# Optimization experiments

Hardware: AMD Instinct MI355X
Metric: run time of the kernel (lower is better)

The kernel has to match this reference:

```python
import jax, jax.numpy as jnp
import numpy as np
from jax import lax

B, T, D, H = 2, 2048, 512, 8
HD = D // H
EPS = 1e-5


def _layernorm(x, g, b):
    m = jnp.mean(x, axis=-1, keepdims=True)
    v = jnp.var(x, axis=-1, keepdims=True)
    return (x - m) / jnp.sqrt(v + EPS) * g + b


def setup_inputs() -> dict:
    key = jax.random.key(0)
    ks = jax.random.split(key, 16)
    s = 0.02
    return {
        "x": jax.random.normal(ks[0], (B, T, D), jnp.float32),
        "pe": jax.random.normal(ks[1], (B, T, D), jnp.float32),
        "conv_w": jax.random.normal(ks[2], (D, D, 3), jnp.float32) * s,   # OIH
        "conv_b": jnp.zeros((D,), jnp.float32),
        "in_proj_w": jax.random.normal(ks[3], (3 * D, D), jnp.float32) * s,
        "in_proj_b": jnp.zeros((3 * D,), jnp.float32),
        "out_proj_w": jax.random.normal(ks[4], (D, D), jnp.float32) * s,
        "out_proj_b": jnp.zeros((D,), jnp.float32),
        "ln1_g": jnp.ones((D,), jnp.float32),
        "ln1_b": jnp.zeros((D,), jnp.float32),
        "w1": jax.random.normal(ks[5], (2 * D, D), jnp.float32) * s,
        "b1": jnp.zeros((2 * D,), jnp.float32),
        "w2": jax.random.normal(ks[6], (D, 2 * D), jnp.float32) * s,
        "b2": jnp.zeros((D,), jnp.float32),
        "ln2_g": jnp.ones((D,), jnp.float32),
        "ln2_b": jnp.zeros((D,), jnp.float32),
    }


def reference(x, pe, conv_w, conv_b, in_proj_w, in_proj_b, out_proj_w,
              out_proj_b, ln1_g, ln1_b, w1, b1, w2, b2, ln2_g, ln2_b):
    Bv, Tv, Dv = x.shape
    window = max(Tv // 4, 1)
    half = window // 2
    idx = jnp.arange(Tv)
    blocked = jnp.abs(idx[:, None] - idx[None, :]) > half  # [T, T]
    mask = jnp.where(blocked, -jnp.inf, 0.0).astype(x.dtype)

    # Conv1d on values: x [B,T,D] -> [B,D,T], kernel3 pad1, back to [B,T,D]
    xT = jnp.transpose(x, (0, 2, 1))
    v_in = lax.conv_general_dilated(xT, conv_w, window_strides=(1,),
                                    padding=((1, 1),),
                                    dimension_numbers=("NCH", "OIH", "NCH"))
    v_in = jnp.transpose(v_in + conv_b[None, :, None], (0, 2, 1))

    # MultiheadAttention(q=x, k=x, v=v_in)
    Wq, Wk, Wv = jnp.split(in_proj_w, 3, axis=0)
    bq, bk, bv = jnp.split(in_proj_b, 3, axis=0)
    q = (x @ Wq.T + bq).reshape(Bv, Tv, H, HD).transpose(0, 2, 1, 3)
    k = (x @ Wk.T + bk).reshape(Bv, Tv, H, HD).transpose(0, 2, 1, 3)
    v = (v_in @ Wv.T + bv).reshape(Bv, Tv, H, HD).transpose(0, 2, 1, 3)

    scores = jnp.einsum("bhqd,bhkd->bhqk", q, k) / np.sqrt(HD).astype(x.dtype)
    scores = scores + mask[None, None]
    attn = jax.nn.softmax(scores, axis=-1)
    ctx = jnp.einsum("bhqk,bhkd->bhqd", attn, v)
    ctx = ctx.transpose(0, 2, 1, 3).reshape(Bv, Tv, Dv)
    attn_out = ctx @ out_proj_w.T + out_proj_b

    h = _layernorm(x + attn_out, ln1_g, ln1_b)
    ffn = jax.nn.relu(h @ w1.T + b1) @ w2.T + b2
    return _layernorm(h + ffn, ln2_g, ln2_b)
```

## Files before the change

kernel.cpp:

```cpp
#include <hip/hip_runtime.h>
#include <cstdint>
#include <cstddef>

static constexpr int kT  = 2048;
static constexpr int kD  = 512;
static constexpr int kB  = 2;
static constexpr int kN  = kB * kT;

using short8 = __attribute__((ext_vector_type(8))) short;
using f32x4  = __attribute__((ext_vector_type(4))) float;
typedef unsigned short ushort;

__device__ inline ushort f2bf(float f) {
  uint32_t u = __builtin_bit_cast(uint32_t, f);
  uint32_t r = (u + 0x7FFFu + ((u >> 16) & 1u)) >> 16;
  return (ushort)r;
}

#define GLOAD_LDS16(g, l)                                         \
  __builtin_amdgcn_global_load_lds(                               \
      (const __attribute__((address_space(1))) void*)(g),         \
      (__attribute__((address_space(3))) void*)(l), 16, 0, 0)

__global__ __launch_bounds__(256) void prep_kernel(
    const float* __restrict__ x,   const float* __restrict__ ipw,
    const float* __restrict__ opw, const float* __restrict__ w1,
    const float* __restrict__ w2,  const float* __restrict__ cw,
    ushort* __restrict__ xb,   ushort* __restrict__ ipwb,
    ushort* __restrict__ opwb, ushort* __restrict__ w1b,
    ushort* __restrict__ w2b,  ushort* __restrict__ wcat,
    ushort* __restrict__ acat)
{
  constexpr int C0 = 524288;
  constexpr int C1 = C0 + 196608;
  constexpr int C2 = C1 + 65536;
  constexpr int C3 = C2 + 131072;
  constexpr int C4 = C3 + 131072;
  constexpr int C5 = C4 + 262144;
  constexpr int C6 = C5 + 786432;

  auto cast4 = [](const float* in, ushort* out, int u) {
    float4 v = *reinterpret_cast<const float4*>(&in[(size_t)u * 4]);
    ushort o[4] = {f2bf(v.x), f2bf(v.y), f2bf(v.z), f2bf(v.w)};
    *reinterpret_cast<uint2*>(&out[(size_t)u * 4]) =
        *reinterpret_cast<uint2*>(o);
  };

  for (int u = blockIdx.x * 256 + threadIdx.x; u < C6; u += gridDim.x * 256) {
    if (u < C0) {
      cast4(x, xb, u);
    } else if (u < C1) {
      cast4(ipw, ipwb, u - C0);
    } else if (u < C2) {
      cast4(opw, opwb, u - C1);
    } else if (u < C3) {
      cast4(w1, w1b, u - C2);
    } else if (u < C4) {
      cast4(w2, w2b, u - C3);
    } else if (u < C5) {
      int t = u - C4;
      int o = t >> 9, i = t & 511;
      const float* src = &cw[(size_t)(o * kD + i) * 3];
      ushort* dst = &wcat[(size_t)o * (3 * kD) + i];
#pragma unroll
      for (int tap = 0; tap < 3; ++tap) dst[tap * kD] = f2bf(src[tap]);
    } else {
      int t = u - C5;
      int m = t / 192, r = t - m * 192;
      int tap = r >> 6, i8 = r & 63;
      int tib = (m & (kT - 1)) + tap - 1;
      ushort ob[8] = {0, 0, 0, 0, 0, 0, 0, 0};
      if (tib >= 0 && tib < kT) {
        const float* src = &x[(size_t)(m + tap - 1) * kD + i8 * 8];
        float4 v0 = *reinterpret_cast<const float4*>(src);
        float4 v1 = *reinterpret_cast<const float4*>(src + 4);
        ob[0] = f2bf(v0.x); ob[1] = f2bf(v0.y); ob[2] = f2bf(v0.z);
        ob[3] = f2bf(v0.w); ob[4] = f2bf(v1.x); ob[5] = f2bf(v1.y);
        ob[6] = f2bf(v1.z); ob[7] = f2bf(v1.w);
      }
      *reinterpret_cast<uint4*>(
          &acat[(size_t)m * (3 * kD) + tap * kD + i8 * 8]) =
          *reinterpret_cast<uint4*>(ob);
    }
  }
}

template <typename OutT, int RELU>
__global__ __launch_bounds__(256) void gemm_bf16(
    const ushort* __restrict__ A, const ushort* __restrict__ W,
    const float* __restrict__ bias, OutT* __restrict__ C,
    int M, int Nn, int K)
{
  __shared__ __align__(16) ushort As[2][64 * 128];
  __shared__ __align__(16) ushort Bs[2][64 * 128];
  const int tid = threadIdx.x;
  const int lane = tid & 63, w = tid >> 6;
  const int wr = w >> 1, wc = w & 1;
  const int m0 = blockIdx.x * 64, n0 = blockIdx.y * 64;
  const int fr = lane & 15, g = lane >> 4;

  f32x4 acc[2][2];
#pragma unroll
  for (int i = 0; i < 2; ++i)
#pragma unroll
    for (int j = 0; j < 2; ++j) acc[i][j] = {0.f, 0.f, 0.f, 0.f};

  const ushort* gA[4];
  const ushort* gB[4];
#pragma unroll
  for (int i = 0; i < 4; ++i) {
    int u = i * 256 + tid;
    int row = u >> 4, c = (u & 15) ^ (row & 7);
    gA[i] = A + (size_t)(m0 + row) * K + c * 8;
    gB[i] = W + (size_t)(n0 + row) * K + c * 8;
  }

  auto stage = [&](int buf, int k0) {
#pragma unroll
    for (int i = 0; i < 4; ++i)
      GLOAD_LDS16(gA[i] + k0, &As[buf][(i * 256 + w * 64) * 8]);
#pragma unroll
    for (int i = 0; i < 4; ++i)
      GLOAD_LDS16(gB[i] + k0, &Bs[buf][(i * 256 + w * 64) * 8]);
  };

  const int nt = K >> 7;
  stage(0, 0);
  for (int t = 0; t < nt; ++t) {
    const int buf = t & 1;
    if (t + 1 < nt) {
      stage(buf ^ 1, (t + 1) << 7);
      asm volatile("s_waitcnt vmcnt(8)" ::: "memory");
    } else {
      asm volatile("s_waitcnt vmcnt(0)" ::: "memory");
    }
    __builtin_amdgcn_s_barrier();
    __builtin_amdgcn_sched_barrier(0);

    short8 a[2][4], b[2][4];
#pragma unroll
    for (int m = 0; m < 2; ++m)
#pragma unroll
      for (int kc = 0; kc < 4; ++kc) {
        int r = wr * 32 + m * 16 + fr;
        a[m][kc] = *reinterpret_cast<const short8*>(
            &As[buf][(r * 16 + ((kc * 4 + g) ^ (r & 7))) * 8]);
      }
#pragma unroll
    for (int n = 0; n < 2; ++n)
#pragma unroll
      for (int kc = 0; kc < 4; ++kc) {
        int r = wc * 32 + n * 16 + fr;
        b[n][kc] = *reinterpret_cast<const short8*>(
            &Bs[buf][(r * 16 + ((kc * 4 + g) ^ (r & 7))) * 8]);
      }
#pragma unroll
    for (int m = 0; m < 2; ++m)
#pragma unroll
      for (int n = 0; n < 2; ++n)
#pragma unroll
        for (int kc = 0; kc < 4; ++kc)
          acc[m][n] = __builtin_amdgcn_mfma_f32_16x16x32_bf16(
              a[m][kc], b[n][kc], acc[m][n], 0, 0, 0);

    __builtin_amdgcn_sched_barrier(0);
    __builtin_amdgcn_s_barrier();
  }

  float bv[2];
#pragma unroll
  for (int n = 0; n < 2; ++n) bv[n] = bias[n0 + wc * 32 + n * 16 + fr];
#pragma unroll
  for (int m = 0; m < 2; ++m) {
#pragma unroll
    for (int j = 0; j < 4; ++j) {
      int row = m0 + wr * 32 + m * 16 + g * 4 + j;
#pragma unroll
      for (int n = 0; n < 2; ++n) {
        int col = n0 + wc * 32 + n * 16 + fr;
        float v = acc[m][n][j] + bv[n];
        if (RELU) v = fmaxf(v, 0.f);
        if constexpr (sizeof(OutT) == 2)
          C[(size_t)row * Nn + col] = (OutT)f2bf(v);
        else
          C[(size_t)row * Nn + col] = (OutT)v;
      }
    }
  }
}

__global__ __launch_bounds__(256) void attn_mfma(
    const ushort* __restrict__ QK, const ushort* __restrict__ V,
    ushort* __restrict__ Ctx)
{
  constexpr int PAD = 72;
  __shared__ __align__(16) ushort Ks[2][64 * 64];
  __shared__ __align__(16) ushort Vt[2][64][PAD];
  __shared__ __align__(16) ushort Pl[4][16][PAD];
  const int tid = threadIdx.x;
  const int lane = tid & 63, w = tid >> 6;
  const int l15 = lane & 15, g = lane >> 4;
  const int bh = blockIdx.y;
  const int b = bh >> 3, h = bh & 7;
  const int r0 = blockIdx.x * 64;
  const int rowbase = b * kT;
  const int qrow0 = r0 + w * 16;
  const int t_lo = max(r0 - 256, 0);
  const int t_last = min(r0 + 256, kT - 64);
  const int ntiles = ((t_last - t_lo) >> 6) + 1;

  short8 qf[2];
  {
    const size_t qb = (size_t)(rowbase + qrow0 + l15) * 1024 + h * 64 + g * 8;
    qf[0] = *reinterpret_cast<const short8*>(&QK[qb]);
    qf[1] = *reinterpret_cast<const short8*>(&QK[qb + 32]);
  }

  uint4 vreg[2];
  auto issueK = [&](int buf, int j0) {
#pragma unroll
    for (int c = 0; c < 2; ++c) {
      int u = c * 256 + tid;
      int row = u >> 3;
      int col8 = (u & 7) ^ (row & 7);
      const ushort* src =
          &QK[(size_t)(rowbase + j0 + row) * 1024 + 512 + h * 64 + col8 * 8];
      GLOAD_LDS16(src, &Ks[buf][(c * 256 + w * 64) * 8]);
    }
  };
  auto issueV = [&](int j0) {
#pragma unroll
    for (int i = 0; i < 2; ++i)
      vreg[i] = *reinterpret_cast<const uint4*>(
          &V[(size_t)(rowbase + j0 + lane) * 512 + h * 64 + (w + 4 * i) * 8]);
  };
  auto writeV = [&](int buf) {
#pragma unroll
    for (int i = 0; i < 2; ++i) {
      int dg = w + 4 * i;
      ushort tmp[8];
      *reinterpret_cast<uint4*>(tmp) = vreg[i];
#pragma unroll
      for (int e = 0; e < 8; ++e) Vt[buf][dg * 8 + e][lane] = tmp[e];
    }
  };

  f32x4 acc[4];
#pragma unroll
  for (int d = 0; d < 4; ++d) acc[d] = {0.f, 0.f, 0.f, 0.f};
  float mrun[4] = {-1e30f, -1e30f, -1e30f, -1e30f};
  float lrun[4] = {0.f, 0.f, 0.f, 0.f};

  issueK(0, t_lo);
  issueV(t_lo);
  asm volatile("s_waitcnt vmcnt(0)" ::: "memory");
  writeV(0);
  __syncthreads();

  for (int tt = 0; tt < ntiles; ++tt) {
    const int buf = tt & 1;
    const int j0 = t_lo + tt * 64;
    if (tt + 1 < ntiles) {
      issueK(buf ^ 1, j0 + 64);
      issueV(j0 + 64);
    }

    f32x4 s[4];
#pragma unroll
    for (int n = 0; n < 4; ++n) {
      f32x4 z = {0.f, 0.f, 0.f, 0.f};
#pragma unroll
      for (int kc = 0; kc < 2; ++kc) {
        int row = n * 16 + l15;
        int unit = row * 8 + ((kc * 4 + g) ^ (row & 7));
        short8 kb = *reinterpret_cast<const short8*>(&Ks[buf][unit * 8]);
        z = __builtin_amdgcn_mfma_f32_16x16x32_bf16(qf[kc], kb, z, 0, 0, 0);
      }
      s[n] = z;
    }
#pragma unroll
    for (int n = 0; n < 4; ++n)
#pragma unroll
      for (int j = 0; j < 4; ++j) {
        int col = j0 + n * 16 + l15;
        int qr = qrow0 + g * 4 + j;
        int dlt = col - qr;
        float v = s[n][j] * 0.125f;
        s[n][j] = (dlt > 256 || dlt < -256) ? -1e30f : v;
      }
    float pn[4][4];
    float sold[4];
#pragma unroll
    for (int j = 0; j < 4; ++j) {
      float mx = fmaxf(fmaxf(s[0][j], s[1][j]), fmaxf(s[2][j], s[3][j]));
      mx = fmaxf(mx, __shfl_xor(mx, 1));
      mx = fmaxf(mx, __shfl_xor(mx, 2));
      mx = fmaxf(mx, __shfl_xor(mx, 4));
      mx = fmaxf(mx, __shfl_xor(mx, 8));
      float mnew = fmaxf(mrun[j], mx);
      float sc = __expf(mrun[j] - mnew);
      mrun[j] = mnew;
      sold[j] = sc;
      float rs = 0.f;
#pragma unroll
      for (int n = 0; n < 4; ++n) {
        float p = __expf(s[n][j] - mnew);
        pn[n][j] = p;
        rs += p;
      }
      rs += __shfl_xor(rs, 1);
      rs += __shfl_xor(rs, 2);
      rs += __shfl_xor(rs, 4);
      rs += __shfl_xor(rs, 8);
      lrun[j] = lrun[j] * sc + rs;
    }
#pragma unroll
    for (int d = 0; d < 4; ++d)
#pragma unroll
      for (int j = 0; j < 4; ++j) acc[d][j] *= sold[j];
#pragma unroll
    for (int n = 0; n < 4; ++n)
#pragma unroll
      for (int j = 0; j < 4; ++j)
        Pl[w][g * 4 + j][n * 16 + l15] = f2bf(pn[n][j]);
    asm volatile("s_waitcnt lgkmcnt(0)" ::: "memory");
    __builtin_amdgcn_sched_barrier(0);

    short8 pa[2];
    pa[0] = *reinterpret_cast<const short8*>(&Pl[w][l15][g * 8]);
    pa[1] = *reinterpret_cast<const short8*>(&Pl[w][l15][32 + g * 8]);
#pragma unroll
    for (int d = 0; d < 4; ++d) {
#pragma unroll
      for (int kc = 0; kc < 2; ++kc) {
        short8 vb = *reinterpret_cast<const short8*>(
            &Vt[buf][d * 16 + l15][kc * 32 + g * 8]);
        acc[d] = __builtin_amdgcn_mfma_f32_16x16x32_bf16(pa[kc], vb, acc[d], 0, 0, 0);
      }
    }

    if (tt + 1 < ntiles) {
      asm volatile("s_waitcnt vmcnt(0)" ::: "memory");
      writeV(buf ^ 1);
    }
    __syncthreads();
  }

  float inv[4];
#pragma unroll
  for (int j = 0; j < 4; ++j) inv[j] = 1.f / lrun[j];
#pragma unroll
  for (int d = 0; d < 4; ++d)
#pragma unroll
    for (int j = 0; j < 4; ++j) {
      float v = acc[d][j] * inv[j];
      Ctx[(size_t)(rowbase + qrow0 + g * 4 + j) * 512 + h * 64 + d * 16 + l15] =
          f2bf(v);
    }
}

__global__ __launch_bounds__(256) void ln_kernel(
    const float* __restrict__ A, const float* __restrict__ Bq,
    const float* __restrict__ G, const float* __restrict__ Bt,
    float* __restrict__ Out, ushort* __restrict__ OutB)
{
  const int lane = threadIdx.x & 63;
  const int wv = threadIdx.x >> 6;
  const int row = blockIdx.x * 4 + wv;
  const size_t base = (size_t)row * kD + lane * 8;

  float4 a0 = *reinterpret_cast<const float4*>(&A[base]);
  float4 a1 = *reinterpret_cast<const float4*>(&A[base + 4]);
  float4 b0 = *reinterpret_cast<const float4*>(&Bq[base]);
  float4 b1 = *reinterpret_cast<const float4*>(&Bq[base + 4]);
  float x[8] = {a0.x + b0.x, a0.y + b0.y, a0.z + b0.z, a0.w + b0.w,
                a1.x + b1.x, a1.y + b1.y, a1.z + b1.z, a1.w + b1.w};
  float s = 0.f, ss = 0.f;
#pragma unroll
  for (int i = 0; i < 8; ++i) { s += x[i]; ss += x[i] * x[i]; }
#pragma unroll
  for (int o = 1; o < 64; o <<= 1) {
    s += __shfl_xor(s, o, 64);
    ss += __shfl_xor(ss, o, 64);
  }
  const float mean = s * (1.f / kD);
  const float var = ss * (1.f / kD) - mean * mean;
  const float rs = rsqrtf(var + 1e-5f);

  const int c = lane * 8;
  float4 g0 = *reinterpret_cast<const float4*>(&G[c]);
  float4 g1 = *reinterpret_cast<const float4*>(&G[c + 4]);
  float4 t0 = *reinterpret_cast<const float4*>(&Bt[c]);
  float4 t1 = *reinterpret_cast<const float4*>(&Bt[c + 4]);
  float y[8];
  y[0] = (x[0] - mean) * rs * g0.x + t0.x;
  y[1] = (x[1] - mean) * rs * g0.y + t0.y;
  y[2] = (x[2] - mean) * rs * g0.z + t0.z;
  y[3] = (x[3] - mean) * rs * g0.w + t0.w;
  y[4] = (x[4] - mean) * rs * g1.x + t1.x;
  y[5] = (x[5] - mean) * rs * g1.y + t1.y;
  y[6] = (x[6] - mean) * rs * g1.z + t1.z;
  y[7] = (x[7] - mean) * rs * g1.w + t1.w;
  *reinterpret_cast<float4*>(&Out[base]) = {y[0], y[1], y[2], y[3]};
  *reinterpret_cast<float4*>(&Out[base + 4]) = {y[4], y[5], y[6], y[7]};
  if (OutB) {
    ushort ob[8];
#pragma unroll
    for (int i = 0; i < 8; ++i) ob[i] = f2bf(y[i]);
    *reinterpret_cast<uint4*>(&OutB[base]) = *reinterpret_cast<uint4*>(ob);
  }
}

extern "C" void kernel_launch(void* const* d_in, const int* in_sizes, int n_in,
                              void* d_out, int out_size, void* d_ws, size_t ws_size,
                              hipStream_t stream)
{
  const float* x   = (const float*)d_in[0];
  const float* cw  = (const float*)d_in[2];
  const float* cb  = (const float*)d_in[3];
  const float* ipw = (const float*)d_in[4];
  const float* ipb = (const float*)d_in[5];
  const float* opw = (const float*)d_in[6];
  const float* opb = (const float*)d_in[7];
  const float* g1  = (const float*)d_in[8];
  const float* b1n = (const float*)d_in[9];
  const float* w1  = (const float*)d_in[10];
  const float* bb1 = (const float*)d_in[11];
  const float* w2  = (const float*)d_in[12];
  const float* bb2 = (const float*)d_in[13];
  const float* g2  = (const float*)d_in[14];
  const float* b2n = (const float*)d_in[15];
  float* out = (float*)d_out;

  char* p = (char*)d_ws;
  auto take = [&](size_t bytes) {
    char* q = p; p += (bytes + 255) & ~size_t(255); return q;
  };
  ushort* xb    = (ushort*)take((size_t)kN * kD * 2);
  char*  acat_r =          take((size_t)kN * 3 * kD * 2);
  ushort* acat  = (ushort*)acat_r;
  ushort* wcat  = (ushort*)take((size_t)kD * 3 * kD * 2);
  ushort* ipwb  = (ushort*)take((size_t)3 * kD * kD * 2);
  ushort* opwb  = (ushort*)take((size_t)kD * kD * 2);
  ushort* w1b   = (ushort*)take((size_t)2 * kD * kD * 2);
  ushort* w2b   = (ushort*)take((size_t)2 * kD * kD * 2);
  ushort* convo = (ushort*)take((size_t)kN * kD * 2);
  char*  qk_r   =          take((size_t)kN * 2 * kD * 2);
  ushort* qkb   = (ushort*)qk_r;
  ushort* vbb   = (ushort*)take((size_t)kN * kD * 2);
  ushort* ctx   = (ushort*)take((size_t)kN * kD * 2);
  float* hbuf   = (float*)take((size_t)kN * kD * 4);
  ushort* hb    = (ushort*)take((size_t)kN * kD * 2);
  float* attno  = (float*)acat_r;
  ushort* f1    = (ushort*)qk_r;
  float* f2     = (float*)acat_r;

  dim3 blk(256);
  prep_kernel<<<dim3(2048), blk, 0, stream>>>(
      x, ipw, opw, w1, w2, cw, xb, ipwb, opwb, w1b, w2b, wcat, acat);

  gemm_bf16<ushort, 0><<<dim3(kN / 64, kD / 64), blk, 0, stream>>>(
      acat, wcat, cb, convo, kN, kD, 3 * kD);
  gemm_bf16<ushort, 0><<<dim3(kN / 64, 1024 / 64), blk, 0, stream>>>(
      xb, ipwb, ipb, qkb, kN, 1024, kD);
  gemm_bf16<ushort, 0><<<dim3(kN / 64, kD / 64), blk, 0, stream>>>(
      convo, ipwb + (size_t)1024 * kD, ipb + 1024, vbb, kN, kD, kD);
  attn_mfma<<<dim3(kT / 64, kB * 8), blk, 0, stream>>>(qkb, vbb, ctx);
  gemm_bf16<float, 0><<<dim3(kN / 64, kD / 64), blk, 0, stream>>>(
      ctx, opwb, opb, attno, kN, kD, kD);
  ln_kernel<<<dim3(kN / 4), blk, 0, stream>>>(x, attno, g1, b1n, hbuf, hb);
  gemm_bf16<ushort, 1><<<dim3(kN / 64, 1024 / 64), blk, 0, stream>>>(
      hb, w1b, bb1, f1, kN, 1024, kD);
  gemm_bf16<float, 0><<<dim3(kN / 64, kD / 64), blk, 0, stream>>>(
      f1, w2b, bb2, f2, kN, kD, 2 * kD);
  ln_kernel<<<dim3(kN / 4), blk, 0, stream>>>(hbuf, f2, g2, b2n, out, nullptr);
}
```

Measured before the change: 204.5 us.

## Fold conv weights into V projection and fuse QK and V GEMMs

```diff
diff --git a/kernel.cpp b/kernel.cpp
--- a/kernel.cpp
+++ b/kernel.cpp
@@ -22,22 +22,29 @@
       (const __attribute__((address_space(1))) void*)(g),         \
       (__attribute__((address_space(3))) void*)(l), 16, 0, 0)
 
+struct __align__(16) SmemGemm {
+  ushort As[2][64 * 128];
+  ushort Bs[2][64 * 128];
+};
+
 __global__ __launch_bounds__(256) void prep_kernel(
     const float* __restrict__ x,   const float* __restrict__ ipw,
     const float* __restrict__ opw, const float* __restrict__ w1,
     const float* __restrict__ w2,  const float* __restrict__ cw,
+    const float* __restrict__ cb,
     ushort* __restrict__ xb,   ushort* __restrict__ ipwb,
     ushort* __restrict__ opwb, ushort* __restrict__ w1b,
-    ushort* __restrict__ w2b,  ushort* __restrict__ wcat,
-    ushort* __restrict__ acat)
+    ushort* __restrict__ w2b,  ushort* __restrict__ wct,
+    ushort* __restrict__ acat, float* __restrict__ bvpart)
 {
   constexpr int C0 = 524288;
   constexpr int C1 = C0 + 196608;
   constexpr int C2 = C1 + 65536;
   constexpr int C3 = C2 + 131072;
   constexpr int C4 = C3 + 131072;
-  constexpr int C5 = C4 + 262144;
+  constexpr int C5 = C4 + 786432;
   constexpr int C6 = C5 + 786432;
+  constexpr int C7 = C6 + 4096;
 
   auto cast4 = [](const float* in, ushort* out, int u) {
     float4 v = *reinterpret_cast<const float4*>(&in[(size_t)u * 4]);
@@ -46,7 +53,7 @@
         *reinterpret_cast<uint2*>(o);
   };
 
-  for (int u = blockIdx.x * 256 + threadIdx.x; u < C6; u += gridDim.x * 256) {
+  for (int u = blockIdx.x * 256 + threadIdx.x; u < C7; u += gridDim.x * 256) {
     if (u < C0) {
       cast4(x, xb, u);
     } else if (u < C1) {
@@ -59,12 +66,10 @@
       cast4(w2, w2b, u - C3);
     } else if (u < C5) {
       int t = u - C4;
-      int o = t >> 9, i = t & 511;
-      const float* src = &cw[(size_t)(o * kD + i) * 3];
-      ushort* dst = &wcat[(size_t)o * (3 * kD) + i];
-#pragma unroll
-      for (int tap = 0; tap < 3; ++tap) dst[tap * kD] = f2bf(src[tap]);
-    } else {
+      int ti = t >> 9, c = t & 511;
+      int tap = ti >> 9, i = ti & 511;
+      wct[(size_t)ti * 512 + c] = f2bf(cw[((size_t)c * 512 + i) * 3 + tap]);
+    } else if (u < C6) {
       int t = u - C5;
       int m = t / 192, r = t - m * 192;
       int tap = r >> 6, i8 = r & 63;
@@ -81,22 +86,28 @@
       *reinterpret_cast<uint4*>(
           &acat[(size_t)m * (3 * kD) + tap * kD + i8 * 8]) =
           *reinterpret_cast<uint4*>(ob);
+    } else {
+      int t = u - C6;
+      int o = t >> 3, seg = t & 7;
+      float s = 0.f;
+      const float* wr = &ipw[(size_t)(1024 + o) * kD + seg * 64];
+      const float* cr = &cb[seg * 64];
+#pragma unroll 8
+      for (int c = 0; c < 64; ++c) s = fmaf(wr[c], cr[c], s);
+      bvpart[t] = s;
     }
   }
 }
 
 template <typename OutT, int RELU>
-__global__ __launch_bounds__(256) void gemm_bf16(
+__device__ void gemm_tile(SmemGemm& S,
     const ushort* __restrict__ A, const ushort* __restrict__ W,
     const float* __restrict__ bias, OutT* __restrict__ C,
-    int M, int Nn, int K)
-{
-  __shared__ __align__(16) ushort As[2][64 * 128];
-  __shared__ __align__(16) ushort Bs[2][64 * 128];
+    int Nn, int K, int m0, int n0)
+{
   const int tid = threadIdx.x;
   const int lane = tid & 63, w = tid >> 6;
   const int wr = w >> 1, wc = w & 1;
-  const int m0 = blockIdx.x * 64, n0 = blockIdx.y * 64;
   const int fr = lane & 15, g = lane >> 4;
 
   f32x4 acc[2][2];
@@ -118,10 +129,10 @@
   auto stage = [&](int buf, int k0) {
 #pragma unroll
     for (int i = 0; i < 4; ++i)
-      GLOAD_LDS16(gA[i] + k0, &As[buf][(i * 256 + w * 64) * 8]);
+      GLOAD_LDS16(gA[i] + k0, &S.As[buf][(i * 256 + w * 64) * 8]);
 #pragma unroll
     for (int i = 0; i < 4; ++i)
-      GLOAD_LDS16(gB[i] + k0, &Bs[buf][(i * 256 + w * 64) * 8]);
+      GLOAD_LDS16(gB[i] + k0, &S.Bs[buf][(i * 256 + w * 64) * 8]);
   };
 
   const int nt = K >> 7;
@@ -137,22 +148,22 @@
     __builtin_amdgcn_s_barrier();
     __builtin_amdgcn_sched_barrier(0);
 
-    short8 a[2][4], b[2][4];
+    short8 av[2][4], bv[2][4];
 #pragma unroll
     for (int m = 0; m < 2; ++m)
 #pragma unroll
       for (int kc = 0; kc < 4; ++kc) {
         int r = wr * 32 + m * 16 + fr;
-        a[m][kc] = *reinterpret_cast<const short8*>(
-            &As[buf][(r * 16 + ((kc * 4 + g) ^ (r & 7))) * 8]);
+        av[m][kc] = *reinterpret_cast<const short8*>(
+            &S.As[buf][(r * 16 + ((kc * 4 + g) ^ (r & 7))) * 8]);
       }
 #pragma unroll
     for (int n = 0; n < 2; ++n)
 #pragma unroll
       for (int kc = 0; kc < 4; ++kc) {
         int r = wc * 32 + n * 16 + fr;
-        b[n][kc] = *reinterpret_cast<const short8*>(
-            &Bs[buf][(r * 16 + ((kc * 4 + g) ^ (r & 7))) * 8]);
+        bv[n][kc] = *reinterpret_cast<const short8*>(
+            &S.Bs[buf][(r * 16 + ((kc * 4 + g) ^ (r & 7))) * 8]);
       }
 #pragma unroll
     for (int m = 0; m < 2; ++m)
@@ -161,15 +172,16 @@
 #pragma unroll
         for (int kc = 0; kc < 4; ++kc)
           acc[m][n] = __builtin_amdgcn_mfma_f32_16x16x32_bf16(
-              a[m][kc], b[n][kc], acc[m][n], 0, 0, 0);
+              av[m][kc], bv[n][kc], acc[m][n], 0, 0, 0);
 
     __builtin_amdgcn_sched_barrier(0);
     __builtin_amdgcn_s_barrier();
   }
 
-  float bv[2];
-#pragma unroll
-  for (int n = 0; n < 2; ++n) bv[n] = bias[n0 + wc * 32 + n * 16 + fr];
+  float bb[2];
+#pragma unroll
+  for (int n = 0; n < 2; ++n)
+    bb[n] = bias ? bias[n0 + wc * 32 + n * 16 + fr] : 0.f;
 #pragma unroll
   for (int m = 0; m < 2; ++m) {
 #pragma unroll
@@ -178,7 +190,7 @@
 #pragma unroll
       for (int n = 0; n < 2; ++n) {
         int col = n0 + wc * 32 + n * 16 + fr;
-        float v = acc[m][n][j] + bv[n];
+        float v = acc[m][n][j] + bb[n];
         if (RELU) v = fmaxf(v, 0.f);
         if constexpr (sizeof(OutT) == 2)
           C[(size_t)row * Nn + col] = (OutT)f2bf(v);
@@ -186,6 +198,53 @@
           C[(size_t)row * Nn + col] = (OutT)v;
       }
     }
+  }
+}
+
+template <typename OutT, int RELU>
+__global__ __launch_bounds__(256) void gemm_bf16(
+    const ushort* __restrict__ A, const ushort* __restrict__ W,
+    const float* __restrict__ bias, OutT* __restrict__ C, int Nn, int K)
+{
+  __shared__ SmemGemm S;
+  gemm_tile<OutT, RELU>(S, A, W, bias, C, Nn, K,
+                        blockIdx.x * 64, blockIdx.y * 64);
+}
+
+__global__ __launch_bounds__(256) void wprep_kernel(
+    const ushort* __restrict__ ipwb, const ushort* __restrict__ wct,
+    ushort* __restrict__ wveff, const float* __restrict__ ipb,
+    const float* __restrict__ bvpart, float* __restrict__ bveff)
+{
+  __shared__ SmemGemm S;
+  const int bid = blockIdx.x;
+  const int m0 = (bid / 24) * 64, n0 = (bid % 24) * 64;
+  gemm_tile<ushort, 0>(S, ipwb + (size_t)1024 * kD, wct, nullptr, wveff,
+                       3 * kD, kD, m0, n0);
+  if (bid < 2) {
+    int o = bid * 256 + threadIdx.x;
+    float s = ipb[1024 + o];
+#pragma unroll
+    for (int e = 0; e < 8; ++e) s += bvpart[o * 8 + e];
+    bveff[o] = s;
+  }
+}
+
+__global__ __launch_bounds__(256) void qkv_kernel(
+    const ushort* __restrict__ xb, const ushort* __restrict__ acat,
+    const ushort* __restrict__ ipwb, const float* __restrict__ ipb,
+    const ushort* __restrict__ wveff, const float* __restrict__ bveff,
+    ushort* __restrict__ qkb, ushort* __restrict__ vbb)
+{
+  __shared__ SmemGemm S;
+  const int bid = blockIdx.x;
+  if (bid < 1024) {
+    gemm_tile<ushort, 0>(S, xb, ipwb, ipb, qkb, 1024, kD,
+                         (bid >> 4) * 64, (bid & 15) * 64);
+  } else {
+    const int t = bid - 1024;
+    gemm_tile<ushort, 0>(S, acat, wveff, bveff, vbb, kD, 3 * kD,
+                         (t >> 3) * 64, (t & 7) * 64);
   }
 }
 
@@ -439,12 +498,14 @@
   ushort* xb    = (ushort*)take((size_t)kN * kD * 2);
   char*  acat_r =          take((size_t)kN * 3 * kD * 2);
   ushort* acat  = (ushort*)acat_r;
-  ushort* wcat  = (ushort*)take((size_t)kD * 3 * kD * 2);
+  ushort* wct   = (ushort*)take((size_t)3 * kD * kD * 2);
+  ushort* wveff = (ushort*)take((size_t)kD * 3 * kD * 2);
   ushort* ipwb  = (ushort*)take((size_t)3 * kD * kD * 2);
   ushort* opwb  = (ushort*)take((size_t)kD * kD * 2);
   ushort* w1b   = (ushort*)take((size_t)2 * kD * kD * 2);
   ushort* w2b   = (ushort*)take((size_t)2 * kD * kD * 2);
-  ushort* convo = (ushort*)take((size_t)kN * kD * 2);
+  float* bvpart = (float*)take(4096 * 4);
+  float* bveff  = (float*)take(512 * 4);
   char*  qk_r   =          take((size_t)kN * 2 * kD * 2);
   ushort* qkb   = (ushort*)qk_r;
   ushort* vbb   = (ushort*)take((size_t)kN * kD * 2);
@@ -457,21 +518,19 @@
 
   dim3 blk(256);
   prep_kernel<<<dim3(2048), blk, 0, stream>>>(
-      x, ipw, opw, w1, w2, cw, xb, ipwb, opwb, w1b, w2b, wcat, acat);
-
-  gemm_bf16<ushort, 0><<<dim3(kN / 64, kD / 64), blk, 0, stream>>>(
-      acat, wcat, cb, convo, kN, kD, 3 * kD);
-  gemm_bf16<ushort, 0><<<dim3(kN / 64, 1024 / 64), blk, 0, stream>>>(
-      xb, ipwb, ipb, qkb, kN, 1024, kD);
-  gemm_bf16<ushort, 0><<<dim3(kN / 64, kD / 64), blk, 0, stream>>>(
-      convo, ipwb + (size_t)1024 * kD, ipb + 1024, vbb, kN, kD, kD);
+      x, ipw, opw, w1, w2, cw, cb,
+      xb, ipwb, opwb, w1b, w2b, wct, acat, bvpart);
+  wprep_kernel<<<dim3(192), blk, 0, stream>>>(
+      ipwb, wct, wveff, ipb, bvpart, bveff);
+  qkv_kernel<<<dim3(1536), blk, 0, stream>>>(
+      xb, acat, ipwb, ipb, wveff, bveff, qkb, vbb);
   attn_mfma<<<dim3(kT / 64, kB * 8), blk, 0, stream>>>(qkb, vbb, ctx);
   gemm_bf16<float, 0><<<dim3(kN / 64, kD / 64), blk, 0, stream>>>(
-      ctx, opwb, opb, attno, kN, kD, kD);
+      ctx, opwb, opb, attno, kD, kD);
   ln_kernel<<<dim3(kN / 4), blk, 0, stream>>>(x, attno, g1, b1n, hbuf, hb);
   gemm_bf16<ushort, 1><<<dim3(kN / 64, 1024 / 64), blk, 0, stream>>>(
-      hb, w1b, bb1, f1, kN, 1024, kD);
+      hb, w1b, bb1, f1, 1024, kD);
   gemm_bf16<float, 0><<<dim3(kN / 64, kD / 64), blk, 0, stream>>>(
-      f1, w2b, bb2, f2, kN, kD, 2 * kD);
+      f1, w2b, bb2, f2, kD, 2 * kD);
   ln_kernel<<<dim3(kN / 4), blk, 0, stream>>>(hbuf, f2, g2, b2n, out, nullptr);
 }
```

Measured after the change: 205.0 us. No clear change (+0.3%).
